# Kernel optimization log

Hardware: AMD Instinct MI355X
Metric: run time of the kernel (lower is better)

## Reference

```python
import jax, jax.numpy as jnp
import numpy as np

K = 9          # kernel points along H (morph=0 -> kernel shape (9,1))
PAD = K // 2   # same padding along H
EPS = 1e-5     # batchnorm eps


def setup_inputs() -> dict:
    key = jax.random.key(0)
    ks = jax.random.split(key, 6)
    B, Cin, Cout, H, W = 4, 64, 64, 160, 160
    x = jax.random.normal(ks[0], (B, Cin, H, W), jnp.float32)
    # offset branch conv: 2*K offset channels, kernel (K,1)
    w_off = jax.random.normal(ks[1], (2 * K, Cin, K, 1), jnp.float32) * 0.05
    b_off = jax.random.normal(ks[2], (2 * K,), jnp.float32) * 0.05
    gamma = jnp.ones((2 * K,), jnp.float32)
    beta = jnp.zeros((2 * K,), jnp.float32)
    # deformable conv weights: kernel (K,1), groups=1
    w_def = jax.random.normal(ks[3], (Cout, Cin, K, 1), jnp.float32) * 0.05
    b_def = jax.random.normal(ks[4], (Cout,), jnp.float32) * 0.05
    return {"x": x, "w_off": w_off, "b_off": b_off, "gamma": gamma,
            "beta": beta, "w_def": w_def, "b_def": b_def}


def _convert_offsets(off):
    # morph=0: even channels (x) -> 0; odd channels (y) -> per-kernel-point cumsum
    c = K // 2
    y = off[:, 1::2]                                            # [B,K,H,W]
    top = jnp.flip(jnp.cumsum(jnp.flip(y[:, :c + 1], 1), 1), 1)  # suffix-cumsum to center
    bot = jnp.cumsum(jnp.concatenate([top[:, c:c + 1], y[:, c + 1:]], 1), 1)
    y_new = jnp.concatenate([top[:, :c], bot], 1)
    return jnp.zeros_like(off).at[:, 1::2].set(y_new)


def _deform_conv(x, off, w, b):
    B, C, H, W = x.shape
    dy = off[:, 0::2]                                           # [B,K,H,W]
    dx = off[:, 1::2]
    ky = jnp.arange(K, dtype=x.dtype).reshape(1, K, 1, 1)
    py = jnp.arange(H, dtype=x.dtype).reshape(1, 1, H, 1) - PAD + ky + dy
    px = jnp.arange(W, dtype=x.dtype).reshape(1, 1, 1, W) + dx
    y0 = jnp.floor(py)
    x0 = jnp.floor(px)
    fy = py - y0
    fx = px - x0
    y0i = y0.astype(jnp.int32)
    x0i = x0.astype(jnp.int32)
    xf = x.reshape(B, C, H * W)

    def gather(yc, xc):
        # zero-padded bilinear corner gather -> [B,C,K,H,W]
        valid = ((yc >= 0) & (yc < H) & (xc >= 0) & (xc < W)).astype(x.dtype)
        lin = jnp.clip(yc, 0, H - 1) * W + jnp.clip(xc, 0, W - 1)
        v = jax.vmap(lambda img, idx: img[:, idx])(xf, lin)
        return v * valid[:, None]

    w00 = ((1 - fy) * (1 - fx))[:, None]
    w01 = ((1 - fy) * fx)[:, None]
    w10 = (fy * (1 - fx))[:, None]
    w11 = (fy * fx)[:, None]
    samples = (w00 * gather(y0i, x0i) + w01 * gather(y0i, x0i + 1)
               + w10 * gather(y0i + 1, x0i) + w11 * gather(y0i + 1, x0i + 1))
    # contract kernel points and input channels
    return jnp.einsum('bckhw,ock->bohw', samples, w[:, :, :, 0]) + b[None, :, None, None]


def reference(x, w_off, b_off, gamma, beta, w_def, b_def):
    # offset branch: conv -> batchnorm (training-mode stats) -> tanh -> snake cumsum
    off = jax.lax.conv_general_dilated(
        x, w_off, (1, 1), ((PAD, PAD), (0, 0)),
        dimension_numbers=('NCHW', 'OIHW', 'NCHW')) + b_off[None, :, None, None]
    mu = off.mean((0, 2, 3), keepdims=True)
    var = off.var((0, 2, 3), keepdims=True)
    off = (off - mu) * jax.lax.rsqrt(var + EPS) * gamma[None, :, None, None] + beta[None, :, None, None]
    off = _convert_offsets(jnp.tanh(off))
    return _deform_conv(x, off, w_def, b_def)
```

## Files before the change

### kernel.cpp

```cpp
#include <hip/hip_runtime.h>
#include <hip/hip_fp16.h>
#include <math.h>

#define HW    25600
#define WID   160
#define HEI   160
#define BB    4
#define CIN   64
#define COUT  64
#define NBN   102400
#define TSTR  162

typedef _Float16 f16x8 __attribute__((ext_vector_type(8)));
typedef float    f32x4 __attribute__((ext_vector_type(4)));

union U4 { int i[4]; f16x8 v; };
union HU { unsigned u; __half2 h; };

__device__ __forceinline__ unsigned short f2h(float f) {
    return __half_as_ushort(__float2half(f));
}

__global__ __launch_bounds__(256) void p0_prep(
        const float* __restrict__ x, const float* __restrict__ w_def,
        const float* __restrict__ w_off,
        unsigned short* __restrict__ xbT, unsigned short* __restrict__ wtA,
        unsigned short* __restrict__ wofA, float* __restrict__ stats) {
    int t = threadIdx.x;
    int blk = blockIdx.x;
    if (blk == 640) {
        for (int u = 0; u < 144; ++u) {
            int idx = t + u * 256;
            int k = idx >> 12;
            int r = idx & 4095;
            int chalf = r >> 11;
            int og = (r >> 9) & 3;
            int L = (r >> 3) & 63;
            int j = idx & 7;
            int o = og * 16 + (L & 15);
            int c = chalf * 32 + (L >> 4) * 8 + j;
            wtA[idx] = f2h(w_def[(o * CIN + c) * 9 + k]);
        }
        for (int u = 0; u < 36; ++u) {
            int idx = t + u * 256;
            int jj = idx & 7;
            int L  = (idx >> 3) & 63;
            int ch = (idx >> 9) & 1;
            int k  = idx >> 10;
            int j  = L & 15;
            int c  = ch * 32 + (L >> 4) * 8 + jj;
            wofA[idx] = (j < 9) ? f2h(w_off[((2 * j + 1) * CIN + c) * 9 + k])
                                : (unsigned short)0;
        }
        if (t < 32) stats[t] = 0.f;
        return;
    }
    __shared__ __align__(16) unsigned short tile[CIN * TSTR];
    int b = blk / HEI, h = blk % HEI;
    const float* xp = x + (b * CIN) * HW + h * WID;
    unsigned* ti = (unsigned*)tile;
#pragma unroll
    for (int u = 0; u < 10; ++u) {
        int e = t + u * 256;
        int c = e / 40, wq = e - c * 40;
        const float4 v = *(const float4*)(xp + c * HW + 4 * wq);
        unsigned p01 = f2h(v.x) | ((unsigned)f2h(v.y) << 16);
        unsigned p23 = f2h(v.z) | ((unsigned)f2h(v.w) << 16);
        ti[81 * c + 2 * wq]     = p01;
        ti[81 * c + 2 * wq + 1] = p23;
    }
    __syncthreads();
    unsigned* dst = (unsigned*)(xbT + (b * HEI + h) * (WID * 64));
#pragma unroll
    for (int u = 0; u < 20; ++u) {
        int e = t + u * 256;
        int w = e >> 5, cp = e & 31;
        unsigned lo = tile[(2 * cp) * TSTR + w];
        unsigned hi = tile[(2 * cp + 1) * TSTR + w];
        dst[e] = lo | (hi << 16);
    }
}

__global__ __launch_bounds__(256) void k1_offconv_mfma(
        const unsigned short* __restrict__ xbT,
        const unsigned short* __restrict__ wofA,
        const float* __restrict__ b_off,
        float* __restrict__ off_odd, float* __restrict__ stats) {
    int t = threadIdx.x;
    int blk = blockIdx.x;
    int xcd = blk & 7;
    int idx = blk >> 3;
    int b = idx / 20;
    int h = xcd * 20 + (idx - b * 20);
    int wave = t >> 6, lane = t & 63;
    int l15 = lane & 15, q = lane >> 4;

    int npx = (wave < 2) ? 3 : 2;
    f32x4 acc[3];
#pragma unroll
    for (int i = 0; i < 3; ++i) acc[i] = (f32x4){0.f, 0.f, 0.f, 0.f};

    int klo = 4 - h;   if (klo < 0) klo = 0;
    int khi = 163 - h; if (khi > 8) khi = 8;

    for (int k = klo; k <= khi; ++k) {
        int py = h + k - 4;
        const unsigned short* row = xbT + (b * HEI + py) * (WID * 64);
        f16x8 a0 = *(const f16x8*)(wofA + ((k * 2 + 0) * 64 + lane) * 8);
        f16x8 a1 = *(const f16x8*)(wofA + ((k * 2 + 1) * 64 + lane) * 8);
#pragma unroll
        for (int u = 0; u < 3; ++u) {
            if (u >= npx) break;
            int px = (wave + u * 4) * 16 + l15;
            const unsigned short* sp = row + px * 64;
            f16x8 b0 = *(const f16x8*)(sp + q * 8);
            f16x8 b1 = *(const f16x8*)(sp + 32 + q * 8);
            acc[u] = __builtin_amdgcn_mfma_f32_16x16x32_f16(a0, b0, acc[u], 0, 0, 0);
            acc[u] = __builtin_amdgcn_mfma_f32_16x16x32_f16(a1, b1, acc[u], 0, 0, 0);
        }
    }

    float sS[4] = {0.f, 0.f, 0.f, 0.f}, sQ[4] = {0.f, 0.f, 0.f, 0.f};
#pragma unroll
    for (int u = 0; u < 3; ++u) {
        if (u >= npx) break;
        int px = (wave + u * 4) * 16 + l15;
#pragma unroll
        for (int r = 0; r < 4; ++r) {
            int j = q * 4 + r;
            if (j < 9) {
                float v = acc[u][r] + b_off[2 * j + 1];
                off_odd[(b * 9 + j) * HW + h * WID + px] = v;
                sS[r] += v; sQ[r] += v * v;
            }
        }
    }
#pragma unroll
    for (int o = 1; o < 16; o <<= 1) {
#pragma unroll
        for (int r = 0; r < 4; ++r) {
            sS[r] += __shfl_xor(sS[r], o);
            sQ[r] += __shfl_xor(sQ[r], o);
        }
    }
    __shared__ float redS[4][16], redQ[4][16];
    if (l15 == 0) {
#pragma unroll
        for (int r = 0; r < 4; ++r) {
            int j = q * 4 + r;
            if (j < 9) { redS[wave][j] = sS[r]; redQ[wave][j] = sQ[r]; }
        }
    }
    __syncthreads();
    if (t < 18) {
        int j = (t < 9) ? t : t - 9;
        float v = (t < 9) ? redS[0][j] + redS[1][j] + redS[2][j] + redS[3][j]
                          : redQ[0][j] + redQ[1][j] + redQ[2][j] + redQ[3][j];
        atomicAdd(&stats[t], v);
    }
}

__global__ __launch_bounds__(256, 5) void k4_deform_mfma(
        const unsigned short* __restrict__ xbT,
        const float* __restrict__ off_odd,
        const float* __restrict__ stats,
        const float* __restrict__ gamma,
        const float* __restrict__ beta,
        const unsigned short* __restrict__ wtA,
        const float* __restrict__ b_def,
        float* __restrict__ out) {
    __shared__ __align__(16) int S[2][80 * 36];
    __shared__ unsigned P0h[9][80], P1h[9][80];
    __shared__ int      PXI[9][80];

    int t   = threadIdx.x;
    int blk = blockIdx.x;
    int xcd = blk & 7;
    int idx = blk >> 3;
    int b   = idx / 40;
    int r2  = idx - b * 40;
    int h   = xcd * 20 + (r2 >> 1);
    int half = r2 & 1;
    int p0  = half * 80;
    int wave = t >> 6, lane = t & 63;
    int l15 = lane & 15, q = lane >> 4;

    if (t < 80) {
        int px = p0 + t;
        float tv[9];
#pragma unroll
        for (int j = 0; j < 9; ++j) {
            float mean = stats[j] * (1.0f / NBN);
            float var  = stats[9 + j] * (1.0f / NBN) - mean * mean;
            float inv  = rsqrtf(var + 1e-5f);
            float v = off_odd[(b * 9 + j) * HW + h * WID + px];
            tv[j] = tanhf((v - mean) * inv * gamma[2 * j + 1] + beta[2 * j + 1]);
        }
        float dxv[9];
        dxv[4] = tv[4];
#pragma unroll
        for (int i = 5; i < 9; ++i) dxv[i] = dxv[i - 1] + tv[i];
#pragma unroll
        for (int i = 3; i >= 0; --i) dxv[i] = dxv[i + 1] + tv[i];
#pragma unroll
        for (int j = 0; j < 9; ++j) {
            float pxf = (float)px + dxv[j];
            float x0f = floorf(pxf);
            float fx  = pxf - x0f;
            int   x0  = (int)x0f;
            float s0f = (x0 >= 0 && x0 < WID) ? 1.f - fx : 0.f;
            float s1f = (x0 >= -1 && x0 < WID - 1) ? fx : 0.f;
            unsigned h0 = f2h(s0f), h1 = f2h(s1f);
            P0h[j][t] = h0 | (h0 << 16);
            P1h[j][t] = h1 | (h1 << 16);
            int xi0 = min(max(x0, 0), WID - 1);
            int xi1 = min(max(x0 + 1, 0), WID - 1);
            PXI[j][t] = xi0 | (xi1 << 16);
        }
    }
    __syncthreads();

    f32x4 acc[5];
#pragma unroll
    for (int i = 0; i < 5; ++i) acc[i] = (f32x4){0.f, 0.f, 0.f, 0.f};

    int klo = 4 - h;   if (klo < 0) klo = 0;
    int khi = 163 - h; if (khi > 8) khi = 8;

    int    A[10], Bv[10];
    f16x8  wpa, wpb;
    int    pxb = t >> 5, ci = t & 31;

#define PF(kk)                                                                  \
    {                                                                           \
        int py = h + (kk) - 4;                                                  \
        const int* row = (const int*)xbT + (b * HEI + py) * (WID * 32);         \
        _Pragma("unroll")                                                       \
        for (int u = 0; u < 10; ++u) {                                          \
            int xi = PXI[kk][pxb + u * 8];                                      \
            A[u]  = row[(xi & 0xffff) * 32 + ci];                               \
            Bv[u] = row[(xi >> 16) * 32 + ci];                                  \
        }                                                                       \
        wpa = *(const f16x8*)(wtA + ((((kk) * 2 + 0) * 4 + wave) * 64 + lane) * 8); \
        wpb = *(const f16x8*)(wtA + ((((kk) * 2 + 1) * 4 + wave) * 64 + lane) * 8); \
    }

    PF(klo);
    int buf = 0;

    for (int k = klo; k <= khi; ++k) {
        int* Sb = S[buf];
#pragma unroll
        for (int u = 0; u < 10; ++u) {
            int pxl = pxb + u * 8;
            HU sa, sb, av, bv, r;
            sa.u = P0h[k][pxl];
            sb.u = P1h[k][pxl];
            av.u = (unsigned)A[u];
            bv.u = (unsigned)Bv[u];
            r.h  = __hfma2(sb.h, bv.h, __hmul2(sa.h, av.h));
            Sb[pxl * 36 + ci] = (int)r.u;
        }
        __syncthreads();

        f16x8 wf0 = wpa, wf1 = wpb;
        if (k < khi) PF(k + 1);

#pragma unroll
        for (int pxt = 0; pxt < 5; ++pxt) {
            const int* sp = &Sb[(pxt * 16 + l15) * 36];
            U4 u0, u1;
            *(int4*)u0.i = *(const int4*)(sp + q * 4);
            *(int4*)u1.i = *(const int4*)(sp + 16 + q * 4);
            acc[pxt] = __builtin_amdgcn_mfma_f32_16x16x32_f16(wf0, u0.v, acc[pxt], 0, 0, 0);
            acc[pxt] = __builtin_amdgcn_mfma_f32_16x16x32_f16(wf1, u1.v, acc[pxt], 0, 0, 0);
        }
        buf ^= 1;
    }
#undef PF

    float bd[4];
#pragma unroll
    for (int r = 0; r < 4; ++r) bd[r] = b_def[wave * 16 + q * 4 + r];
#pragma unroll
    for (int pxt = 0; pxt < 5; ++pxt) {
#pragma unroll
        for (int r = 0; r < 4; ++r) {
            int o = wave * 16 + q * 4 + r;
            out[(b * COUT + o) * HW + h * WID + p0 + pxt * 16 + l15] = acc[pxt][r] + bd[r];
        }
    }
}

extern "C" void kernel_launch(void* const* d_in, const int* in_sizes, int n_in,
                              void* d_out, int out_size, void* d_ws, size_t ws_size,
                              hipStream_t stream) {
    const float* x     = (const float*)d_in[0];
    const float* w_off = (const float*)d_in[1];
    const float* b_off = (const float*)d_in[2];
    const float* gamma = (const float*)d_in[3];
    const float* beta  = (const float*)d_in[4];
    const float* w_def = (const float*)d_in[5];
    const float* b_def = (const float*)d_in[6];
    float* out = (float*)d_out;

    float* off_odd       = (float*)d_ws;
    float* stats         = off_odd + 921600;
    unsigned short* wtA  = (unsigned short*)(stats + 32);
    unsigned short* wofA = wtA + 36864;
    unsigned short* xbT  = wofA + 9216;

    p0_prep<<<641, 256, 0, stream>>>(x, w_def, w_off, xbT, wtA, wofA, stats);
    k1_offconv_mfma<<<640, 256, 0, stream>>>(xbT, wofA, b_off, off_odd, stats);
    k4_deform_mfma<<<1280, 256, 0, stream>>>(xbT, off_odd, stats, gamma, beta,
                                             wtA, b_def, out);
}
```

Baseline: 155.7 us.

## Split offset conv finer, vectorize deform gathers, use fast tanh, drop row-bound loop

The offset conv kernel now runs 1280 blocks of 5 waves, each wave handling a single 16-pixel tile, instead of 640 blocks with uneven per-wave pixel counts. The deform kernel gathers 16-byte int4 chunks per corner instead of 4-byte words, and does the half-precision bilinear blend on four words per thread with one vector LDS store. Out-of-range rows are handled by zeroing the bilinear weights and clamping the row index, so all 9 kernel points always run with a uniform loop. tanhf is replaced by an exp2/rcp approximation, which costs some accuracy and does redundant work on border rows.

```diff
diff --git a/kernel.cpp b/kernel.cpp
--- a/kernel.cpp
+++ b/kernel.cpp
@@ -19,6 +19,11 @@
 
 __device__ __forceinline__ unsigned short f2h(float f) {
     return __half_as_ushort(__float2half(f));
+}
+
+__device__ __forceinline__ float ftanh(float x) {
+    float e = __builtin_amdgcn_exp2f(x * 2.8853900817779268f);
+    return 1.0f - 2.0f * __builtin_amdgcn_rcpf(e + 1.0f);
 }
 
 __global__ __launch_bounds__(256) void p0_prep(
@@ -81,7 +86,7 @@
     }
 }
 
-__global__ __launch_bounds__(256) void k1_offconv_mfma(
+__global__ __launch_bounds__(320) void k1_offconv_mfma(
         const unsigned short* __restrict__ xbT,
         const unsigned short* __restrict__ wofA,
         const float* __restrict__ b_off,
@@ -90,49 +95,38 @@
     int blk = blockIdx.x;
     int xcd = blk & 7;
     int idx = blk >> 3;
-    int b = idx / 20;
-    int h = xcd * 20 + (idx - b * 20);
+    int b   = idx / 40;
+    int r2  = idx - b * 40;
+    int h   = xcd * 20 + (r2 >> 1);
+    int p0  = (r2 & 1) * 80;
     int wave = t >> 6, lane = t & 63;
     int l15 = lane & 15, q = lane >> 4;
-
-    int npx = (wave < 2) ? 3 : 2;
-    f32x4 acc[3];
-#pragma unroll
-    for (int i = 0; i < 3; ++i) acc[i] = (f32x4){0.f, 0.f, 0.f, 0.f};
+    int px  = p0 + wave * 16 + l15;
+
+    f32x4 acc = (f32x4){0.f, 0.f, 0.f, 0.f};
 
     int klo = 4 - h;   if (klo < 0) klo = 0;
     int khi = 163 - h; if (khi > 8) khi = 8;
 
     for (int k = klo; k <= khi; ++k) {
         int py = h + k - 4;
-        const unsigned short* row = xbT + (b * HEI + py) * (WID * 64);
+        const unsigned short* sp = xbT + (b * HEI + py) * (WID * 64) + px * 64;
         f16x8 a0 = *(const f16x8*)(wofA + ((k * 2 + 0) * 64 + lane) * 8);
         f16x8 a1 = *(const f16x8*)(wofA + ((k * 2 + 1) * 64 + lane) * 8);
-#pragma unroll
-        for (int u = 0; u < 3; ++u) {
-            if (u >= npx) break;
-            int px = (wave + u * 4) * 16 + l15;
-            const unsigned short* sp = row + px * 64;
-            f16x8 b0 = *(const f16x8*)(sp + q * 8);
-            f16x8 b1 = *(const f16x8*)(sp + 32 + q * 8);
-            acc[u] = __builtin_amdgcn_mfma_f32_16x16x32_f16(a0, b0, acc[u], 0, 0, 0);
-            acc[u] = __builtin_amdgcn_mfma_f32_16x16x32_f16(a1, b1, acc[u], 0, 0, 0);
-        }
+        f16x8 b0 = *(const f16x8*)(sp + q * 8);
+        f16x8 b1 = *(const f16x8*)(sp + 32 + q * 8);
+        acc = __builtin_amdgcn_mfma_f32_16x16x32_f16(a0, b0, acc, 0, 0, 0);
+        acc = __builtin_amdgcn_mfma_f32_16x16x32_f16(a1, b1, acc, 0, 0, 0);
     }
 
     float sS[4] = {0.f, 0.f, 0.f, 0.f}, sQ[4] = {0.f, 0.f, 0.f, 0.f};
 #pragma unroll
-    for (int u = 0; u < 3; ++u) {
-        if (u >= npx) break;
-        int px = (wave + u * 4) * 16 + l15;
-#pragma unroll
-        for (int r = 0; r < 4; ++r) {
-            int j = q * 4 + r;
-            if (j < 9) {
-                float v = acc[u][r] + b_off[2 * j + 1];
-                off_odd[(b * 9 + j) * HW + h * WID + px] = v;
-                sS[r] += v; sQ[r] += v * v;
-            }
+    for (int r = 0; r < 4; ++r) {
+        int j = q * 4 + r;
+        if (j < 9) {
+            float v = acc[r] + b_off[2 * j + 1];
+            off_odd[(b * 9 + j) * HW + h * WID + px] = v;
+            sS[r] = v; sQ[r] = v * v;
         }
     }
 #pragma unroll
@@ -143,7 +137,7 @@
             sQ[r] += __shfl_xor(sQ[r], o);
         }
     }
-    __shared__ float redS[4][16], redQ[4][16];
+    __shared__ float redS[5][16], redQ[5][16];
     if (l15 == 0) {
 #pragma unroll
         for (int r = 0; r < 4; ++r) {
@@ -154,8 +148,10 @@
     __syncthreads();
     if (t < 18) {
         int j = (t < 9) ? t : t - 9;
-        float v = (t < 9) ? redS[0][j] + redS[1][j] + redS[2][j] + redS[3][j]
-                          : redQ[0][j] + redQ[1][j] + redQ[2][j] + redQ[3][j];
+        float v = 0.f;
+#pragma unroll
+        for (int w = 0; w < 5; ++w)
+            v += (t < 9) ? redS[w][j] : redQ[w][j];
         atomicAdd(&stats[t], v);
     }
 }
@@ -180,8 +176,7 @@
     int b   = idx / 40;
     int r2  = idx - b * 40;
     int h   = xcd * 20 + (r2 >> 1);
-    int half = r2 & 1;
-    int p0  = half * 80;
+    int p0  = (r2 & 1) * 80;
     int wave = t >> 6, lane = t & 63;
     int l15 = lane & 15, q = lane >> 4;
 
@@ -194,7 +189,7 @@
             float var  = stats[9 + j] * (1.0f / NBN) - mean * mean;
             float inv  = rsqrtf(var + 1e-5f);
             float v = off_odd[(b * 9 + j) * HW + h * WID + px];
-            tv[j] = tanhf((v - mean) * inv * gamma[2 * j + 1] + beta[2 * j + 1]);
+            tv[j] = ftanh((v - mean) * inv * gamma[2 * j + 1] + beta[2 * j + 1]);
         }
         float dxv[9];
         dxv[4] = tv[4];
@@ -204,12 +199,14 @@
         for (int i = 3; i >= 0; --i) dxv[i] = dxv[i + 1] + tv[i];
 #pragma unroll
         for (int j = 0; j < 9; ++j) {
+            int py = h + j - 4;
+            bool rowok = (py >= 0) && (py < HEI);
             float pxf = (float)px + dxv[j];
             float x0f = floorf(pxf);
             float fx  = pxf - x0f;
             int   x0  = (int)x0f;
-            float s0f = (x0 >= 0 && x0 < WID) ? 1.f - fx : 0.f;
-            float s1f = (x0 >= -1 && x0 < WID - 1) ? fx : 0.f;
+            float s0f = (rowok && x0 >= 0 && x0 < WID) ? 1.f - fx : 0.f;
+            float s1f = (rowok && x0 >= -1 && x0 < WID - 1) ? fx : 0.f;
             unsigned h0 = f2h(s0f), h1 = f2h(s1f);
             P0h[j][t] = h0 | (h0 << 16);
             P1h[j][t] = h1 | (h1 << 16);
@@ -224,47 +221,57 @@
 #pragma unroll
     for (int i = 0; i < 5; ++i) acc[i] = (f32x4){0.f, 0.f, 0.f, 0.f};
 
-    int klo = 4 - h;   if (klo < 0) klo = 0;
-    int khi = 163 - h; if (khi > 8) khi = 8;
-
-    int    A[10], Bv[10];
-    f16x8  wpa, wpb;
-    int    pxb = t >> 5, ci = t & 31;
+    int4     A4[3], B4[3];
+    unsigned sa[3], sb[3];
+    f16x8    wpa, wpb;
 
 #define PF(kk)                                                                  \
     {                                                                           \
-        int py = h + (kk) - 4;                                                  \
-        const int* row = (const int*)xbT + (b * HEI + py) * (WID * 32);         \
+        int pyc = min(max(h + (kk) - 4, 0), HEI - 1);                           \
+        const int4* rowI4 = (const int4*)(xbT + (b * HEI + pyc) * (WID * 64));  \
         _Pragma("unroll")                                                       \
-        for (int u = 0; u < 10; ++u) {                                          \
-            int xi = PXI[kk][pxb + u * 8];                                      \
-            A[u]  = row[(xi & 0xffff) * 32 + ci];                               \
-            Bv[u] = row[(xi >> 16) * 32 + ci];                                  \
+        for (int u = 0; u < 3; ++u) {                                           \
+            if (u < 2 || t < 128) {                                             \
+                int id = t + u * 256;                                           \
+                int pxl = id >> 3, c4 = id & 7;                                 \
+                int xi = PXI[kk][pxl];                                          \
+                sa[u] = P0h[kk][pxl];                                           \
+                sb[u] = P1h[kk][pxl];                                           \
+                A4[u] = rowI4[(xi & 0xffff) * 8 + c4];                          \
+                B4[u] = rowI4[(xi >> 16) * 8 + c4];                             \
+            }                                                                   \
         }                                                                       \
         wpa = *(const f16x8*)(wtA + ((((kk) * 2 + 0) * 4 + wave) * 64 + lane) * 8); \
         wpb = *(const f16x8*)(wtA + ((((kk) * 2 + 1) * 4 + wave) * 64 + lane) * 8); \
     }
 
-    PF(klo);
+    PF(0);
     int buf = 0;
 
-    for (int k = klo; k <= khi; ++k) {
+    for (int k = 0; k < 9; ++k) {
         int* Sb = S[buf];
 #pragma unroll
-        for (int u = 0; u < 10; ++u) {
-            int pxl = pxb + u * 8;
-            HU sa, sb, av, bv, r;
-            sa.u = P0h[k][pxl];
-            sb.u = P1h[k][pxl];
-            av.u = (unsigned)A[u];
-            bv.u = (unsigned)Bv[u];
-            r.h  = __hfma2(sb.h, bv.h, __hmul2(sa.h, av.h));
-            Sb[pxl * 36 + ci] = (int)r.u;
+        for (int u = 0; u < 3; ++u) {
+            if (u < 2 || t < 128) {
+                int id = t + u * 256;
+                int pxl = id >> 3, c4 = id & 7;
+                HU sah, sbh; sah.u = sa[u]; sbh.u = sb[u];
+                int4 r4;
+                HU a, bb, r;
+#pragma unroll
+                for (int ii = 0; ii < 4; ++ii) {
+                    a.u  = (unsigned)(&A4[u].x)[ii];
+                    bb.u = (unsigned)(&B4[u].x)[ii];
+                    r.h  = __hfma2(sbh.h, bb.h, __hmul2(sah.h, a.h));
+                    (&r4.x)[ii] = (int)r.u;
+                }
+                *(int4*)(Sb + pxl * 36 + (c4 << 2)) = r4;
+            }
         }
         __syncthreads();
 
         f16x8 wf0 = wpa, wf1 = wpb;
-        if (k < khi) PF(k + 1);
+        if (k < 8) PF(k + 1);
 
 #pragma unroll
         for (int pxt = 0; pxt < 5; ++pxt) {
@@ -311,7 +318,7 @@
     unsigned short* xbT  = wofA + 9216;
 
     p0_prep<<<641, 256, 0, stream>>>(x, w_def, w_off, xbT, wtA, wofA, stats);
-    k1_offconv_mfma<<<640, 256, 0, stream>>>(xbT, wofA, b_off, off_odd, stats);
+    k1_offconv_mfma<<<1280, 320, 0, stream>>>(xbT, wofA, b_off, off_odd, stats);
     k4_deform_mfma<<<1280, 256, 0, stream>>>(xbT, off_odd, stats, gamma, beta,
                                              wtA, b_def, out);
 }
```

Result: no change. 153.1 us (-1.6%).
